# Optimization experiments

Hardware: AMD Instinct MI355X
Metric: run time of the kernel (lower is better)

The kernel has to match this reference:

```python
import jax, jax.numpy as jnp
import numpy as np

N_NODES = 50000
N_EDGES = 600000
N_GRAPHS = 512
D = 128          # in_channels == hidden_channels
L = 4            # num_layers (total GINConv count)
N_CLASSES = 10
BN_EPS = 1e-5


def setup_inputs() -> dict:
    key = jax.random.key(0)
    ks = jax.random.split(key, 12)
    x = jax.random.normal(ks[0], (N_NODES, D), dtype=jnp.float32)
    edge_index = jax.random.randint(ks[1], (2, N_EDGES), 0, N_NODES, dtype=jnp.int64)
    batch = jnp.sort(jax.random.randint(ks[2], (N_NODES,), 0, N_GRAPHS, dtype=jnp.int64))
    s = 1.0 / np.sqrt(D)
    W1 = jax.random.uniform(ks[3], (L, D, D), jnp.float32, -s, s)
    b1 = jax.random.uniform(ks[4], (L, D), jnp.float32, -s, s)
    W2 = jax.random.uniform(ks[5], (L, D, D), jnp.float32, -s, s)
    b2 = jax.random.uniform(ks[6], (L, D), jnp.float32, -s, s)
    eps = jnp.zeros((L,), jnp.float32)            # train_eps=True, init 0
    gamma = jnp.ones((L, D), jnp.float32)
    beta = jnp.zeros((L, D), jnp.float32)
    sl = 1.0 / np.sqrt(D * L)
    Wlin = jax.random.uniform(ks[7], (D * L, N_CLASSES), jnp.float32, -sl, sl)
    blin = jax.random.uniform(ks[8], (N_CLASSES,), jnp.float32, -sl, sl)
    return {"x": x, "edge_index": edge_index, "batch": batch,
            "W1": W1, "b1": b1, "W2": W2, "b2": b2, "eps": eps,
            "gamma": gamma, "beta": beta, "Wlin": Wlin, "blin": blin}


def reference(x, edge_index, batch, W1, b1, W2, b2, eps, gamma, beta, Wlin, blin):
    src, dst = edge_index[0], edge_index[1]
    h = x
    pools = []
    for l in range(L):
        # GINConv: sum-aggregate neighbor features at dst, add (1+eps)*self
        agg = jax.ops.segment_sum(h[src], dst, num_segments=N_NODES)
        z = (1.0 + eps[l]) * h + agg
        # 2-layer MLP
        z = jnp.maximum(z @ W1[l] + b1[l], 0.0) @ W2[l] + b2[l]
        # BatchNorm1d (training mode: batch stats, biased variance)
        mean = jnp.mean(z, axis=0)
        var = jnp.mean(jnp.square(z - mean), axis=0)
        z = (z - mean) * jax.lax.rsqrt(var + BN_EPS) * gamma[l] + beta[l]
        h = jnp.maximum(z, 0.0)
        # global_add_pool per graph
        pools.append(jax.ops.segment_sum(h, batch, num_segments=N_GRAPHS))
    x_cat = jnp.concatenate(pools, axis=1)  # [N_GRAPHS, D*L]
    return x_cat @ Wlin + blin              # dropout = identity (eval)
```

## Files before the change

kernel.cpp:

```cpp
#include <hip/hip_runtime.h>

#define N_NODES 50000
#define N_EDGES 600000
#define N_GRAPHS 512
#define DIM 128
#define NLAYERS 4
#define NCLASSES 10
#define KPD 132

typedef __attribute__((ext_vector_type(8))) short short8;
typedef __attribute__((ext_vector_type(4))) float f32x4;

union Frag { short8 s; uint4 u; };

__device__ inline unsigned short f2bf(float v) {
    union { float f; unsigned u; } c; c.f = v;
    unsigned u = c.u;
    u += 0x7FFFu + ((u >> 16) & 1u);
    return (unsigned short)(u >> 16);
}
__device__ inline float bf2f(unsigned short h) {
    union { float f; unsigned u; } c; c.u = ((unsigned)h) << 16;
    return c.f;
}
__device__ inline float bfu_lo(unsigned u) {
    union { float f; unsigned x; } c; c.x = u << 16; return c.f;
}
__device__ inline float bfu_hi(unsigned u) {
    union { float f; unsigned x; } c; c.x = u & 0xFFFF0000u; return c.f;
}
__device__ inline void addRow(float* acc, const uint4& v) {
    acc[0] += bfu_lo(v.x); acc[1] += bfu_hi(v.x);
    acc[2] += bfu_lo(v.y); acc[3] += bfu_hi(v.y);
    acc[4] += bfu_lo(v.z); acc[5] += bfu_hi(v.z);
    acc[6] += bfu_lo(v.w); acc[7] += bfu_hi(v.w);
}

__global__ __launch_bounds__(256) void hist_kernel(
    const int* __restrict__ dst, int* __restrict__ deg)
{
    int e = blockIdx.x * 256 + threadIdx.x;
    if (e >= N_EDGES) return;
    atomicAdd(&deg[dst[e]], 1);
}

__global__ __launch_bounds__(256) void scan1_kernel(
    const int* __restrict__ deg, int* __restrict__ bsum)
{
    __shared__ int red[256];
    int t = threadIdx.x;
    int i4 = blockIdx.x * 256 + t;
    int s = 0;
    if (i4 < 12500) {
        int4 v = ((const int4*)deg)[i4];
        s = v.x + v.y + v.z + v.w;
    }
    red[t] = s;
    __syncthreads();
    for (int off = 128; off > 0; off >>= 1) {
        if (t < off) red[t] += red[t + off];
        __syncthreads();
    }
    if (t == 0) bsum[blockIdx.x] = red[0];
}

__global__ __launch_bounds__(64) void scan2_kernel(int* __restrict__ bsum)
{
    __shared__ int sh[64];
    int t = threadIdx.x;
    sh[t] = (t < 49) ? bsum[t] : 0;
    __syncthreads();
    if (t == 0) {
        int run = 0;
        for (int i = 0; i < 49; i++) { int v = sh[i]; sh[i] = run; run += v; }
    }
    __syncthreads();
    if (t < 49) bsum[t] = sh[t];
}

__global__ __launch_bounds__(256) void scan3_kernel(
    const int* __restrict__ deg, const int* __restrict__ bsum,
    int* __restrict__ rowptr, int* __restrict__ cursor)
{
    __shared__ int red[256];
    int t = threadIdx.x;
    int i4 = blockIdx.x * 256 + t;
    int4 v = {0, 0, 0, 0};
    if (i4 < 12500) v = ((const int4*)deg)[i4];
    int s = v.x + v.y + v.z + v.w;
    red[t] = s;
    __syncthreads();
    for (int off = 1; off < 256; off <<= 1) {
        int val = (t >= off) ? red[t - off] : 0;
        __syncthreads();
        red[t] += val;
        __syncthreads();
    }
    int run = bsum[blockIdx.x] + (t ? red[t - 1] : 0);
    if (i4 < 12500) {
        int4 rp;
        rp.x = run; run += v.x;
        rp.y = run; run += v.y;
        rp.z = run; run += v.z;
        rp.w = run; run += v.w;
        ((int4*)rowptr)[i4] = rp;
        ((int4*)cursor)[i4] = rp;
    }
    if (blockIdx.x == 0 && t == 0) rowptr[N_NODES] = N_EDGES;
}

__global__ __launch_bounds__(256) void fill_kernel(
    const int* __restrict__ src, const int* __restrict__ dst,
    int* __restrict__ cursor, int* __restrict__ csr)
{
    int e = blockIdx.x * 256 + threadIdx.x;
    if (e >= N_EDGES) return;
    int p = atomicAdd(&cursor[dst[e]], 1);
    csr[p] = src[e];
}

__global__ __launch_bounds__(256) void bounds_kernel(
    const int* __restrict__ batch, int* __restrict__ gstart)
{
    int n = blockIdx.x * 256 + threadIdx.x;
    if (n >= N_NODES) return;
    int b = batch[n];
    int bp = (n == 0) ? -1 : batch[n - 1];
    for (int g = bp + 1; g <= b; g++) gstart[g] = n;
    if (n == N_NODES - 1)
        for (int g = b + 1; g <= N_GRAPHS; g++) gstart[g] = N_NODES;
}

__global__ __launch_bounds__(256) void xconv_kernel(
    const float* __restrict__ x, unsigned int* __restrict__ xb)
{
    int idx = blockIdx.x * 256 + threadIdx.x;
    if (idx >= N_NODES * 32) return;
    float4 v = ((const float4*)x)[idx];
    uint2 o;
    o.x = (unsigned)f2bf(v.x) | ((unsigned)f2bf(v.y) << 16);
    o.y = (unsigned)f2bf(v.z) | ((unsigned)f2bf(v.w) << 16);
    ((uint2*)xb)[idx] = o;
}

__global__ __launch_bounds__(256) void wconv_kernel(
    const float* __restrict__ W1, const float* __restrict__ W2,
    unsigned short* __restrict__ whi)
{
    int idx = blockIdx.x * 256 + threadIdx.x;
    if (idx >= NLAYERS * 2 * 16384) return;
    int f   = idx & 16383;
    int w01 = (idx >> 14) & 1;
    int l   = idx >> 15;
    int j    = f & 7;
    int lane = (f >> 3) & 63;
    int cg   = (f >> 9) & 7;
    int ks   = f >> 12;
    int k = ks * 32 + (lane >> 4) * 8 + j;
    int n = cg * 16 + (lane & 15);
    const float* W = (w01 == 0 ? W1 : W2) + (size_t)l * 16384;
    whi[idx] = f2bf(W[k * 128 + n]);
}

__global__ __launch_bounds__(256, 2) void gin_layer_kernel(
    const unsigned int* __restrict__ hb,
    const int* __restrict__ rowptr, const int* __restrict__ csr,
    const float* __restrict__ epsP,
    float* __restrict__ z,
    const unsigned short* __restrict__ whi,
    const float* __restrict__ b1, const float* __restrict__ b2,
    float* __restrict__ stats)
{
    __shared__ unsigned int tpk[64 * KPD];

    const int t = threadIdx.x;
    const int lane = t & 63;
    const int w = t >> 6;
    const int wr = w & 1, wc = w >> 1;
    const int l15 = lane & 15, quad = lane >> 4;
    const int base = blockIdx.x * 64;

    {
        const int m = t >> 2;
        const int c = t & 3;
        const int n = base + m;
        const uint4* hb4 = (const uint4*)hb;
        float acc[32];
        #pragma unroll
        for (int i = 0; i < 32; i++) acc[i] = 0.f;
        if (n < N_NODES) {
            const float e1 = 1.0f + epsP[0];
            const uint4* self = hb4 + (size_t)n * 16 + c * 4;
            #pragma unroll
            for (int j = 0; j < 4; j++) {
                uint4 v = self[j];
                float* a = acc + j * 8;
                a[0] = e1 * bfu_lo(v.x); a[1] = e1 * bfu_hi(v.x);
                a[2] = e1 * bfu_lo(v.y); a[3] = e1 * bfu_hi(v.y);
                a[4] = e1 * bfu_lo(v.z); a[5] = e1 * bfu_hi(v.z);
                a[6] = e1 * bfu_lo(v.w); a[7] = e1 * bfu_hi(v.w);
            }
            int beg = rowptr[n], end = rowptr[n + 1];
            int e = beg;
            for (; e + 1 < end; e += 2) {
                int s0 = csr[e], s1 = csr[e + 1];
                const uint4* r0 = hb4 + (size_t)s0 * 16 + c * 4;
                const uint4* r1 = hb4 + (size_t)s1 * 16 + c * 4;
                uint4 a0 = r0[0], a1 = r0[1], a2 = r0[2], a3 = r0[3];
                uint4 b0 = r1[0], b1v = r1[1], b2v = r1[2], b3 = r1[3];
                addRow(acc + 0, a0);  addRow(acc + 8, a1);
                addRow(acc + 16, a2); addRow(acc + 24, a3);
                addRow(acc + 0, b0);  addRow(acc + 8, b1v);
                addRow(acc + 16, b2v); addRow(acc + 24, b3);
            }
            if (e < end) {
                int s0 = csr[e];
                const uint4* r0 = hb4 + (size_t)s0 * 16 + c * 4;
                uint4 a0 = r0[0], a1 = r0[1], a2 = r0[2], a3 = r0[3];
                addRow(acc + 0, a0);  addRow(acc + 8, a1);
                addRow(acc + 16, a2); addRow(acc + 24, a3);
            }
        }
        unsigned int* dp = &tpk[m * KPD + c * 32];
        #pragma unroll
        for (int i = 0; i < 32; i++) {
            unsigned short h = f2bf(acc[i]);
            unsigned short lo = f2bf(acc[i] - bf2f(h));
            dp[i] = (unsigned)h | ((unsigned)lo << 16);
        }
    }
    __syncthreads();

    f32x4 acc[2][4];
    #pragma unroll
    for (int s = 0; s < 2; s++)
        #pragma unroll
        for (int i = 0; i < 4; i++) acc[s][i] = (f32x4){0.f, 0.f, 0.f, 0.f};

    const int arowd0 = (32 * wr + l15) * KPD;
    const int arowd1 = arowd0 + 16 * KPD;

    #pragma unroll
    for (int kh = 0; kh < 2; kh++) {
        Frag bf[2][4];
        uint4 u00[2], u01[2], u10[2], u11[2];
        #pragma unroll
        for (int kk = 0; kk < 2; kk++) {
            int ks = kh * 2 + kk;
            #pragma unroll
            for (int i = 0; i < 4; i++) {
                size_t woff = (size_t)(((ks * 8 + wc * 4 + i) * 64 + lane) * 8);
                bf[kk][i].s = *((const short8*)&whi[woff]);
            }
            int kd = ks * 32 + quad * 8;
            u00[kk] = *((uint4*)&tpk[arowd0 + kd]);
            u01[kk] = *((uint4*)&tpk[arowd0 + kd + 4]);
            u10[kk] = *((uint4*)&tpk[arowd1 + kd]);
            u11[kk] = *((uint4*)&tpk[arowd1 + kd + 4]);
        }
        #pragma unroll
        for (int kk = 0; kk < 2; kk++) {
            Frag ah0, al0, ah1, al1;
            ah0.u = (uint4){ (u00[kk].x & 0xFFFFu) | (u00[kk].y << 16),
                             (u00[kk].z & 0xFFFFu) | (u00[kk].w << 16),
                             (u01[kk].x & 0xFFFFu) | (u01[kk].y << 16),
                             (u01[kk].z & 0xFFFFu) | (u01[kk].w << 16) };
            al0.u = (uint4){ (u00[kk].x >> 16) | (u00[kk].y & 0xFFFF0000u),
                             (u00[kk].z >> 16) | (u00[kk].w & 0xFFFF0000u),
                             (u01[kk].x >> 16) | (u01[kk].y & 0xFFFF0000u),
                             (u01[kk].z >> 16) | (u01[kk].w & 0xFFFF0000u) };
            ah1.u = (uint4){ (u10[kk].x & 0xFFFFu) | (u10[kk].y << 16),
                             (u10[kk].z & 0xFFFFu) | (u10[kk].w << 16),
                             (u11[kk].x & 0xFFFFu) | (u11[kk].y << 16),
                             (u11[kk].z & 0xFFFFu) | (u11[kk].w << 16) };
            al1.u = (uint4){ (u10[kk].x >> 16) | (u10[kk].y & 0xFFFF0000u),
                             (u10[kk].z >> 16) | (u10[kk].w & 0xFFFF0000u),
                             (u11[kk].x >> 16) | (u11[kk].y & 0xFFFF0000u),
                             (u11[kk].z >> 16) | (u11[kk].w & 0xFFFF0000u) };
            #pragma unroll
            for (int i = 0; i < 4; i++) {
                acc[0][i] = __builtin_amdgcn_mfma_f32_16x16x32_bf16(al0.s, bf[kk][i].s, acc[0][i], 0, 0, 0);
                acc[0][i] = __builtin_amdgcn_mfma_f32_16x16x32_bf16(ah0.s, bf[kk][i].s, acc[0][i], 0, 0, 0);
                acc[1][i] = __builtin_amdgcn_mfma_f32_16x16x32_bf16(al1.s, bf[kk][i].s, acc[1][i], 0, 0, 0);
                acc[1][i] = __builtin_amdgcn_mfma_f32_16x16x32_bf16(ah1.s, bf[kk][i].s, acc[1][i], 0, 0, 0);
            }
        }
    }
    __syncthreads();

    #pragma unroll
    for (int i = 0; i < 4; i++) {
        int col = wc * 64 + i * 16 + l15;
        float bb = b1[col];
        #pragma unroll
        for (int s = 0; s < 2; s++) {
            #pragma unroll
            for (int r = 0; r < 4; r++) {
                int m = 32 * wr + 16 * s + quad * 4 + r;
                float v = fmaxf(acc[s][i][r] + bb, 0.f);
                unsigned short h = f2bf(v);
                unsigned short lo2 = f2bf(v - bf2f(h));
                tpk[m * KPD + col] = (unsigned)h | ((unsigned)lo2 << 16);
            }
            acc[s][i] = (f32x4){0.f, 0.f, 0.f, 0.f};
        }
    }
    __syncthreads();

    const unsigned short* w2 = whi + 16384;
    #pragma unroll
    for (int kh = 0; kh < 2; kh++) {
        Frag bf[2][4];
        uint4 u00[2], u01[2], u10[2], u11[2];
        #pragma unroll
        for (int kk = 0; kk < 2; kk++) {
            int ks = kh * 2 + kk;
            #pragma unroll
            for (int i = 0; i < 4; i++) {
                size_t woff = (size_t)(((ks * 8 + wc * 4 + i) * 64 + lane) * 8);
                bf[kk][i].s = *((const short8*)&w2[woff]);
            }
            int kd = ks * 32 + quad * 8;
            u00[kk] = *((uint4*)&tpk[arowd0 + kd]);
            u01[kk] = *((uint4*)&tpk[arowd0 + kd + 4]);
            u10[kk] = *((uint4*)&tpk[arowd1 + kd]);
            u11[kk] = *((uint4*)&tpk[arowd1 + kd + 4]);
        }
        #pragma unroll
        for (int kk = 0; kk < 2; kk++) {
            Frag ah0, al0, ah1, al1;
            ah0.u = (uint4){ (u00[kk].x & 0xFFFFu) | (u00[kk].y << 16),
                             (u00[kk].z & 0xFFFFu) | (u00[kk].w << 16),
                             (u01[kk].x & 0xFFFFu) | (u01[kk].y << 16),
                             (u01[kk].z & 0xFFFFu) | (u01[kk].w << 16) };
            al0.u = (uint4){ (u00[kk].x >> 16) | (u00[kk].y & 0xFFFF0000u),
                             (u00[kk].z >> 16) | (u00[kk].w & 0xFFFF0000u),
                             (u01[kk].x >> 16) | (u01[kk].y & 0xFFFF0000u),
                             (u01[kk].z >> 16) | (u01[kk].w & 0xFFFF0000u) };
            ah1.u = (uint4){ (u10[kk].x & 0xFFFFu) | (u10[kk].y << 16),
                             (u10[kk].z & 0xFFFFu) | (u10[kk].w << 16),
                             (u11[kk].x & 0xFFFFu) | (u11[kk].y << 16),
                             (u11[kk].z & 0xFFFFu) | (u11[kk].w << 16) };
            al1.u = (uint4){ (u10[kk].x >> 16) | (u10[kk].y & 0xFFFF0000u),
                             (u10[kk].z >> 16) | (u10[kk].w & 0xFFFF0000u),
                             (u11[kk].x >> 16) | (u11[kk].y & 0xFFFF0000u),
                             (u11[kk].z >> 16) | (u11[kk].w & 0xFFFF0000u) };
            #pragma unroll
            for (int i = 0; i < 4; i++) {
                acc[0][i] = __builtin_amdgcn_mfma_f32_16x16x32_bf16(al0.s, bf[kk][i].s, acc[0][i], 0, 0, 0);
                acc[0][i] = __builtin_amdgcn_mfma_f32_16x16x32_bf16(ah0.s, bf[kk][i].s, acc[0][i], 0, 0, 0);
                acc[1][i] = __builtin_amdgcn_mfma_f32_16x16x32_bf16(al1.s, bf[kk][i].s, acc[1][i], 0, 0, 0);
                acc[1][i] = __builtin_amdgcn_mfma_f32_16x16x32_bf16(ah1.s, bf[kk][i].s, acc[1][i], 0, 0, 0);
            }
        }
    }
    __syncthreads();

    float colsum[4], colsq[4];
    #pragma unroll
    for (int i = 0; i < 4; i++) {
        int col = wc * 64 + i * 16 + l15;
        float bb = b2[col];
        float su = 0.f, q2 = 0.f;
        #pragma unroll
        for (int s = 0; s < 2; s++) {
            #pragma unroll
            for (int r = 0; r < 4; r++) {
                int n = base + 32 * wr + 16 * s + quad * 4 + r;
                float v = acc[s][i][r] + bb;
                if (n < N_NODES) {
                    z[(size_t)n * 128 + col] = v;
                    su += v; q2 += v * v;
                }
            }
        }
        colsum[i] = su; colsq[i] = q2;
    }

    float* sums = (float*)tpk;
    float* sqs  = (float*)tpk + 1024;
    #pragma unroll
    for (int i = 0; i < 4; i++) {
        sums[(w * 4 + i) * 64 + lane] = colsum[i];
        sqs [(w * 4 + i) * 64 + lane] = colsq[i];
    }
    __syncthreads();
    if (t < 128) {
        int c = t;
        int wcc = c >> 6, ci = (c >> 4) & 3, cl = c & 15;
        float s = 0.f, q2 = 0.f;
        #pragma unroll
        for (int wrr = 0; wrr < 2; wrr++) {
            int ww = wcc * 2 + wrr;
            #pragma unroll
            for (int u = 0; u < 4; u++) {
                int ln = cl + u * 16;
                s  += sums[(ww * 4 + ci) * 64 + ln];
                q2 += sqs [(ww * 4 + ci) * 64 + ln];
            }
        }
        unsafeAtomicAdd(&stats[c], s);
        unsafeAtomicAdd(&stats[128 + c], q2);
    }
}

__global__ __launch_bounds__(256) void bnpool_kernel(
    const float* __restrict__ z, const float* __restrict__ stats,
    const float* __restrict__ gamma, const float* __restrict__ beta,
    const int* __restrict__ gstart, unsigned int* __restrict__ hout,
    float* __restrict__ pools, int layer)
{
    __shared__ float red[8][128];
    const int g = blockIdx.x;
    const int t = threadIdx.x;
    const int q = t & 31, r = t >> 5;
    const int beg = gstart[g], end = gstart[g + 1];

    float4 s  = ((const float4*)stats)[q];
    float4 sq = ((const float4*)stats)[32 + q];
    float4 gm = ((const float4*)gamma)[q];
    float4 bt = ((const float4*)beta)[q];
    const float invN = 1.0f / (float)N_NODES;
    float m, vr;
    float4 scl, sh;
    m = s.x * invN; vr = sq.x * invN - m * m; scl.x = gm.x * rsqrtf(vr + 1e-5f); sh.x = bt.x - m * scl.x;
    m = s.y * invN; vr = sq.y * invN - m * m; scl.y = gm.y * rsqrtf(vr + 1e-5f); sh.y = bt.y - m * scl.y;
    m = s.z * invN; vr = sq.z * invN - m * m; scl.z = gm.z * rsqrtf(vr + 1e-5f); sh.z = bt.z - m * scl.z;
    m = s.w * invN; vr = sq.w * invN - m * m; scl.w = gm.w * rsqrtf(vr + 1e-5f); sh.w = bt.w - m * scl.w;

    float4 acc = {0.f, 0.f, 0.f, 0.f};
    for (int n = beg + r; n < end; n += 8) {
        float4 zv = ((const float4*)z)[(size_t)n * 32 + q];
        float4 hv;
        hv.x = fmaxf(zv.x * scl.x + sh.x, 0.f);
        hv.y = fmaxf(zv.y * scl.y + sh.y, 0.f);
        hv.z = fmaxf(zv.z * scl.z + sh.z, 0.f);
        hv.w = fmaxf(zv.w * scl.w + sh.w, 0.f);
        uint2 p;
        p.x = (unsigned)f2bf(hv.x) | ((unsigned)f2bf(hv.y) << 16);
        p.y = (unsigned)f2bf(hv.z) | ((unsigned)f2bf(hv.w) << 16);
        ((uint2*)hout)[(size_t)n * 32 + q] = p;
        acc.x += hv.x; acc.y += hv.y; acc.z += hv.z; acc.w += hv.w;
    }
    red[r][q * 4 + 0] = acc.x;
    red[r][q * 4 + 1] = acc.y;
    red[r][q * 4 + 2] = acc.z;
    red[r][q * 4 + 3] = acc.w;
    __syncthreads();
    if (t < 128) {
        float sm = 0.f;
        #pragma unroll
        for (int rr = 0; rr < 8; rr++) sm += red[rr][t];
        pools[(size_t)g * (DIM * NLAYERS) + (size_t)layer * DIM + t] = sm;
    }
}

__global__ __launch_bounds__(64) void final_kernel(
    const float* __restrict__ pools, const float* __restrict__ Wlin,
    const float* __restrict__ blin, float* __restrict__ out)
{
    int g = blockIdx.x;
    int lane = threadIdx.x;
    const float* xr = pools + (size_t)g * (DIM * NLAYERS);
    float a[NCLASSES];
    #pragma unroll
    for (int o = 0; o < NCLASSES; o++) a[o] = 0.f;
    for (int kk = 0; kk < DIM * NLAYERS; kk += 64) {
        float xv = xr[kk + lane];
        const float* wr = Wlin + (size_t)(kk + lane) * NCLASSES;
        #pragma unroll
        for (int o = 0; o < NCLASSES; o++) a[o] += xv * wr[o];
    }
    #pragma unroll
    for (int o = 0; o < NCLASSES; o++) {
        float v = a[o];
        #pragma unroll
        for (int off = 32; off > 0; off >>= 1) v += __shfl_down(v, off, 64);
        if (lane == 0) out[(size_t)g * NCLASSES + o] = v + blin[o];
    }
}

extern "C" void kernel_launch(void* const* d_in, const int* in_sizes, int n_in,
                              void* d_out, int out_size, void* d_ws, size_t ws_size,
                              hipStream_t stream)
{
    const float* x     = (const float*)d_in[0];
    const int*   src   = (const int*)d_in[1];
    const int*   dst   = ((const int*)d_in[1]) + N_EDGES;
    const int*   batch = (const int*)d_in[2];
    const float* W1    = (const float*)d_in[3];
    const float* b1    = (const float*)d_in[4];
    const float* W2    = (const float*)d_in[5];
    const float* b2    = (const float*)d_in[6];
    const float* eps   = (const float*)d_in[7];
    const float* gamma = (const float*)d_in[8];
    const float* beta  = (const float*)d_in[9];
    const float* Wlin  = (const float*)d_in[10];
    const float* blin  = (const float*)d_in[11];
    float* out = (float*)d_out;

    char* ws = (char*)d_ws;
    const size_t FEATF = (size_t)N_NODES * DIM * sizeof(float);
    const size_t FEATH = (size_t)N_NODES * DIM * sizeof(unsigned short);
    size_t off = 0;
    unsigned int* buf_h = (unsigned int*)(ws + off); off += FEATH;
    float* buf_z  = (float*)(ws + off); off += FEATF;
    float* pools  = (float*)(ws + off); off += (size_t)N_GRAPHS * DIM * NLAYERS * sizeof(float);
    float* stats  = (float*)(ws + off); off += (size_t)NLAYERS * 256 * sizeof(float);
    int*   deg    = (int*)(ws + off);   off += (size_t)N_NODES * sizeof(int);
    int*   rowptr = (int*)(ws + off);   off += (size_t)(N_NODES + 1) * sizeof(int) + 12;
    int*   csr    = (int*)(ws + off);   off += (size_t)N_EDGES * sizeof(int);
    int*   gstart = (int*)(ws + off);   off += 2064;
    int*   bsum   = (int*)(ws + off);   off += 208;
    unsigned short* whi = (unsigned short*)(ws + off); off += (size_t)NLAYERS * 2 * 16384 * 2;

    hipMemsetAsync(stats, 0, (size_t)NLAYERS * 256 * sizeof(float), stream);
    hipMemsetAsync(deg, 0, (size_t)N_NODES * sizeof(int), stream);

    hist_kernel<<<(N_EDGES + 255) / 256, 256, 0, stream>>>(dst, deg);
    scan1_kernel<<<49, 256, 0, stream>>>(deg, bsum);
    scan2_kernel<<<1, 64, 0, stream>>>(bsum);
    scan3_kernel<<<49, 256, 0, stream>>>(deg, bsum, rowptr, deg );
    fill_kernel<<<(N_EDGES + 255) / 256, 256, 0, stream>>>(src, dst, deg, csr);
    bounds_kernel<<<(N_NODES + 255) / 256, 256, 0, stream>>>(batch, gstart);
    xconv_kernel<<<(N_NODES * 32 + 255) / 256, 256, 0, stream>>>(x, buf_h);
    wconv_kernel<<<(NLAYERS * 2 * 16384 + 255) / 256, 256, 0, stream>>>(W1, W2, whi);

    for (int l = 0; l < NLAYERS; l++) {
        gin_layer_kernel<<<(N_NODES + 63) / 64, 256, 0, stream>>>(
            buf_h, rowptr, csr, eps + l, buf_z,
            whi + (size_t)l * 32768,
            b1 + (size_t)l * DIM, b2 + (size_t)l * DIM,
            stats + (size_t)l * 256);
        bnpool_kernel<<<N_GRAPHS, 256, 0, stream>>>(
            buf_z, stats + (size_t)l * 256,
            gamma + (size_t)l * DIM, beta + (size_t)l * DIM,
            gstart, buf_h, pools, l);
    }
    final_kernel<<<N_GRAPHS, 64, 0, stream>>>(pools, Wlin, blin, out);
}
```

Baseline: 418.7 us.

## Store pre-BN activations as bf16 via shared-memory staging and unroll gather

The intermediate z buffer between the layer kernel and the BN/pool kernel changes from fp32 to bf16. Values are staged through shared memory so the global store is coalesced, while the BN statistics are still accumulated in fp32 before rounding. The change also unrolls the neighbour gather by four, vectorises the LDS pack store, and drops the occupancy hint from launch_bounds. This halves z write and read traffic, at the cost of rounding z to bf16 before normalisation, which adds some numerical error.

```diff
diff --git a/kernel.cpp b/kernel.cpp
--- a/kernel.cpp
+++ b/kernel.cpp
@@ -162,11 +162,11 @@
     whi[idx] = f2bf(W[k * 128 + n]);
 }
 
-__global__ __launch_bounds__(256, 2) void gin_layer_kernel(
+__global__ __launch_bounds__(256) void gin_layer_kernel(
     const unsigned int* __restrict__ hb,
     const int* __restrict__ rowptr, const int* __restrict__ csr,
     const float* __restrict__ epsP,
-    float* __restrict__ z,
+    unsigned short* __restrict__ z,
     const unsigned short* __restrict__ whi,
     const float* __restrict__ b1, const float* __restrict__ b2,
     float* __restrict__ stats)
@@ -202,18 +202,22 @@
             }
             int beg = rowptr[n], end = rowptr[n + 1];
             int e = beg;
-            for (; e + 1 < end; e += 2) {
-                int s0 = csr[e], s1 = csr[e + 1];
+            for (; e + 3 < end; e += 4) {
+                int s0 = csr[e], s1 = csr[e + 1], s2 = csr[e + 2], s3 = csr[e + 3];
                 const uint4* r0 = hb4 + (size_t)s0 * 16 + c * 4;
                 const uint4* r1 = hb4 + (size_t)s1 * 16 + c * 4;
-                uint4 a0 = r0[0], a1 = r0[1], a2 = r0[2], a3 = r0[3];
-                uint4 b0 = r1[0], b1v = r1[1], b2v = r1[2], b3 = r1[3];
-                addRow(acc + 0, a0);  addRow(acc + 8, a1);
-                addRow(acc + 16, a2); addRow(acc + 24, a3);
-                addRow(acc + 0, b0);  addRow(acc + 8, b1v);
-                addRow(acc + 16, b2v); addRow(acc + 24, b3);
-            }
-            if (e < end) {
+                const uint4* r2 = hb4 + (size_t)s2 * 16 + c * 4;
+                const uint4* r3 = hb4 + (size_t)s3 * 16 + c * 4;
+                uint4 v00 = r0[0], v01 = r0[1], v02 = r0[2], v03 = r0[3];
+                uint4 v10 = r1[0], v11 = r1[1], v12 = r1[2], v13 = r1[3];
+                uint4 v20 = r2[0], v21 = r2[1], v22 = r2[2], v23 = r2[3];
+                uint4 v30 = r3[0], v31 = r3[1], v32 = r3[2], v33 = r3[3];
+                addRow(acc + 0, v00); addRow(acc + 8, v01); addRow(acc + 16, v02); addRow(acc + 24, v03);
+                addRow(acc + 0, v10); addRow(acc + 8, v11); addRow(acc + 16, v12); addRow(acc + 24, v13);
+                addRow(acc + 0, v20); addRow(acc + 8, v21); addRow(acc + 16, v22); addRow(acc + 24, v23);
+                addRow(acc + 0, v30); addRow(acc + 8, v31); addRow(acc + 16, v32); addRow(acc + 24, v33);
+            }
+            for (; e < end; e++) {
                 int s0 = csr[e];
                 const uint4* r0 = hb4 + (size_t)s0 * 16 + c * 4;
                 uint4 a0 = r0[0], a1 = r0[1], a2 = r0[2], a3 = r0[3];
@@ -221,12 +225,19 @@
                 addRow(acc + 16, a2); addRow(acc + 24, a3);
             }
         }
-        unsigned int* dp = &tpk[m * KPD + c * 32];
-        #pragma unroll
-        for (int i = 0; i < 32; i++) {
-            unsigned short h = f2bf(acc[i]);
-            unsigned short lo = f2bf(acc[i] - bf2f(h));
-            dp[i] = (unsigned)h | ((unsigned)lo << 16);
+        uint4* dp = (uint4*)&tpk[m * KPD + c * 32];
+        #pragma unroll
+        for (int v4 = 0; v4 < 8; v4++) {
+            uint4 pk;
+            unsigned* pp = (unsigned*)&pk;
+            #pragma unroll
+            for (int j = 0; j < 4; j++) {
+                float vv = acc[v4 * 4 + j];
+                unsigned short h = f2bf(vv);
+                unsigned short lo = f2bf(vv - bf2f(h));
+                pp[j] = (unsigned)h | ((unsigned)lo << 16);
+            }
+            dp[v4] = pk;
         }
     }
     __syncthreads();
@@ -356,35 +367,47 @@
     }
     __syncthreads();
 
-    float colsum[4], colsq[4];
-    #pragma unroll
-    for (int i = 0; i < 4; i++) {
-        int col = wc * 64 + i * 16 + l15;
-        float bb = b2[col];
-        float su = 0.f, q2 = 0.f;
-        #pragma unroll
-        for (int s = 0; s < 2; s++) {
-            #pragma unroll
-            for (int r = 0; r < 4; r++) {
-                int n = base + 32 * wr + 16 * s + quad * 4 + r;
-                float v = acc[s][i][r] + bb;
-                if (n < N_NODES) {
-                    z[(size_t)n * 128 + col] = v;
-                    su += v; q2 += v * v;
+    unsigned short* zs = (unsigned short*)tpk;
+    float* sums = (float*)((char*)tpk + 20480);
+    float* sqs  = sums + 1024;
+    {
+        float colsum[4], colsq[4];
+        #pragma unroll
+        for (int i = 0; i < 4; i++) {
+            int col = wc * 64 + i * 16 + l15;
+            float bb = b2[col];
+            float su = 0.f, q2 = 0.f;
+            #pragma unroll
+            for (int s = 0; s < 2; s++) {
+                #pragma unroll
+                for (int r = 0; r < 4; r++) {
+                    int m = 32 * wr + 16 * s + quad * 4 + r;
+                    int n = base + m;
+                    float v = acc[s][i][r] + bb;
+                    zs[m * 136 + col] = f2bf(v);
+                    if (n < N_NODES) { su += v; q2 += v * v; }
                 }
             }
-        }
-        colsum[i] = su; colsq[i] = q2;
-    }
-
-    float* sums = (float*)tpk;
-    float* sqs  = (float*)tpk + 1024;
-    #pragma unroll
-    for (int i = 0; i < 4; i++) {
-        sums[(w * 4 + i) * 64 + lane] = colsum[i];
-        sqs [(w * 4 + i) * 64 + lane] = colsq[i];
-    }
-    __syncthreads();
+            colsum[i] = su; colsq[i] = q2;
+        }
+        #pragma unroll
+        for (int i = 0; i < 4; i++) {
+            sums[(w * 4 + i) * 64 + lane] = colsum[i];
+            sqs [(w * 4 + i) * 64 + lane] = colsq[i];
+        }
+    }
+    __syncthreads();
+
+    {
+        int m2 = t >> 2, c2 = t & 3;
+        int n2 = base + m2;
+        if (n2 < N_NODES) {
+            const uint4* srcp = (const uint4*)(zs + m2 * 136 + c2 * 32);
+            uint4* dstp = (uint4*)z + (size_t)n2 * 16 + c2 * 4;
+            #pragma unroll
+            for (int j = 0; j < 4; j++) dstp[j] = srcp[j];
+        }
+    }
     if (t < 128) {
         int c = t;
         int wcc = c >> 6, ci = (c >> 4) & 3, cl = c & 15;
@@ -405,7 +428,7 @@
 }
 
 __global__ __launch_bounds__(256) void bnpool_kernel(
-    const float* __restrict__ z, const float* __restrict__ stats,
+    const unsigned int* __restrict__ z, const float* __restrict__ stats,
     const float* __restrict__ gamma, const float* __restrict__ beta,
     const int* __restrict__ gstart, unsigned int* __restrict__ hout,
     float* __restrict__ pools, int layer)
@@ -430,12 +453,12 @@
 
     float4 acc = {0.f, 0.f, 0.f, 0.f};
     for (int n = beg + r; n < end; n += 8) {
-        float4 zv = ((const float4*)z)[(size_t)n * 32 + q];
+        uint2 zp = ((const uint2*)z)[(size_t)n * 32 + q];
         float4 hv;
-        hv.x = fmaxf(zv.x * scl.x + sh.x, 0.f);
-        hv.y = fmaxf(zv.y * scl.y + sh.y, 0.f);
-        hv.z = fmaxf(zv.z * scl.z + sh.z, 0.f);
-        hv.w = fmaxf(zv.w * scl.w + sh.w, 0.f);
+        hv.x = fmaxf(bfu_lo(zp.x) * scl.x + sh.x, 0.f);
+        hv.y = fmaxf(bfu_hi(zp.x) * scl.y + sh.y, 0.f);
+        hv.z = fmaxf(bfu_lo(zp.y) * scl.z + sh.z, 0.f);
+        hv.w = fmaxf(bfu_hi(zp.y) * scl.w + sh.w, 0.f);
         uint2 p;
         p.x = (unsigned)f2bf(hv.x) | ((unsigned)f2bf(hv.y) << 16);
         p.y = (unsigned)f2bf(hv.z) | ((unsigned)f2bf(hv.w) << 16);
@@ -500,11 +523,10 @@
     float* out = (float*)d_out;
 
     char* ws = (char*)d_ws;
-    const size_t FEATF = (size_t)N_NODES * DIM * sizeof(float);
     const size_t FEATH = (size_t)N_NODES * DIM * sizeof(unsigned short);
     size_t off = 0;
     unsigned int* buf_h = (unsigned int*)(ws + off); off += FEATH;
-    float* buf_z  = (float*)(ws + off); off += FEATF;
+    unsigned short* buf_z = (unsigned short*)(ws + off); off += FEATH;
     float* pools  = (float*)(ws + off); off += (size_t)N_GRAPHS * DIM * NLAYERS * sizeof(float);
     float* stats  = (float*)(ws + off); off += (size_t)NLAYERS * 256 * sizeof(float);
     int*   deg    = (int*)(ws + off);   off += (size_t)N_NODES * sizeof(int);
@@ -533,7 +555,7 @@
             b1 + (size_t)l * DIM, b2 + (size_t)l * DIM,
             stats + (size_t)l * 256);
         bnpool_kernel<<<N_GRAPHS, 256, 0, stream>>>(
-            buf_z, stats + (size_t)l * 256,
+            (const unsigned int*)buf_z, stats + (size_t)l * 256,
             gamma + (size_t)l * DIM, beta + (size_t)l * DIM,
             gstart, buf_h, pools, l);
     }
```

Measured after the change: 422.8 us. No clear change (+1.0%).
